# Kernel tuning notes

Hardware: AMD Instinct MI355X
Metric: run time of the kernel (lower is better)

The kernel has to match this reference:

```python
import jax, jax.numpy as jnp
import numpy as np

B, N, D, C = 2, 65536, 128, 128          # batch, n_entries, input_dim, channel_dim
DEG, N_ACTIVE, STRIDE = 16, 4096, 16     # ring-neighbor sparse structure


def _build_indices():
    """Replicates the original module's Python intersection loops exactly,
    flattening them into (src_i, src_j, pair_out) gather/scatter index arrays.
    k[:, e, :] = sum_m a[:, i_th[m], :] * b[:, j_th[m], :] for each write slot e.
    Each slot e is written exactly once, so scatter-add == the original set."""
    neigh = [[] for _ in range(N)]
    for t in range(N_ACTIVE):
        i = t * STRIDE
        neigh[i] = [((t + dlt) % N_ACTIVE) * STRIDE for dlt in range(1, DEG + 1)]
    src_i, src_j, out = [], [], []
    e = 0
    for i in range(N):
        if not neigh[i]:
            continue
        i_element = list(neigh[i]) + [i]
        i_set = set(i_element)
        for j in neigh[i]:
            j_list = neigh[j]
            j_set = set(j_list)
            j_th = [m for m in j_list if m in i_set]      # order of j's list
            i_th = [m for m in i_element if m in j_set]   # order of i_element
            for ai, bi in zip(i_th, j_th):
                src_i.append(ai)
                src_j.append(bi)
                out.append(e)
            e += 1
    return (np.asarray(src_i, np.int32), np.asarray(src_j, np.int32),
            np.asarray(out, np.int32))


def setup_inputs() -> dict:
    key = jax.random.key(0)
    ks = jax.random.split(key, 8)
    s = 1.0 / np.sqrt(D)
    src_i, src_j, pair_out = _build_indices()
    return {
        "x": jax.random.normal(ks[0], (B, N, D), jnp.float32),
        "ln_in_w": jnp.ones((D,), jnp.float32),
        "ln_in_b": jnp.zeros((D,), jnp.float32),
        "Wla": jax.random.normal(ks[1], (C, D), jnp.float32) * s,
        "bla": jnp.zeros((C,), jnp.float32),
        "Wga": jax.random.normal(ks[2], (C, D), jnp.float32) * s,
        "bga": jnp.zeros((C,), jnp.float32),
        "Wlb": jax.random.normal(ks[3], (C, D), jnp.float32) * s,
        "blb": jnp.zeros((C,), jnp.float32),
        "Wgb": jax.random.normal(ks[4], (C, D), jnp.float32) * s,
        "bgb": jnp.zeros((C,), jnp.float32),
        "ln_o_w": jnp.ones((C,), jnp.float32),
        "ln_o_b": jnp.zeros((C,), jnp.float32),
        "Wgo": jax.random.normal(ks[5], (D, D), jnp.float32) * s,
        "bgo": jnp.zeros((D,), jnp.float32),
        "Wlo": jax.random.normal(ks[6], (D, C), jnp.float32) * s,
        "blo": jnp.zeros((D,), jnp.float32),
        "src_i": jnp.asarray(src_i),
        "src_j": jnp.asarray(src_j),
        "pair_out": jnp.asarray(pair_out),
    }


def _layernorm(x, w, b, eps=1e-5):
    mu = jnp.mean(x, axis=-1, keepdims=True)
    var = jnp.mean(jnp.square(x - mu), axis=-1, keepdims=True)
    return (x - mu) * jax.lax.rsqrt(var + eps) * w + b


def reference(x, ln_in_w, ln_in_b, Wla, bla, Wga, bga, Wlb, blb, Wgb, bgb,
              ln_o_w, ln_o_b, Wgo, bgo, Wlo, blo, src_i, src_j, pair_out):
    xn = _layernorm(x, ln_in_w, ln_in_b)                              # [B,N,D]
    a = jax.nn.sigmoid(xn @ Wga.T + bga) * (xn @ Wla.T + bla)         # [B,N,C]
    b = jax.nn.sigmoid(xn @ Wgb.T + bgb) * (xn @ Wlb.T + blb)         # [B,N,C]
    # triangular update: gather-multiply-sum-scatter over precomputed pairs
    prod = a[:, src_i, :] * b[:, src_j, :]                            # [B,P,C]
    k = jnp.zeros_like(a).at[:, pair_out, :].add(prod)                # [B,N,C]
    out = jax.nn.sigmoid(xn @ Wgo.T + bgo) * (_layernorm(k, ln_o_w, ln_o_b) @ Wlo.T + blo)
    return out
```

## Files before the change

kernel.cpp:

```cpp
#include <hip/hip_runtime.h>


#define BB 2
#define NN 65536
#define DD 128
#define CC 128
#define NA 4096
#define STR 16
#define WSZ 16384

typedef short short8v __attribute__((ext_vector_type(8)));
typedef __bf16 bf16x8 __attribute__((ext_vector_type(8)));
typedef _Float16 f16x2 __attribute__((ext_vector_type(2)));
typedef _Float16 f16x8 __attribute__((ext_vector_type(8)));
typedef __fp16 fp16x2 __attribute__((ext_vector_type(2)));
typedef float f32x4 __attribute__((ext_vector_type(4)));
typedef float f32x2 __attribute__((ext_vector_type(2)));

__device__ __forceinline__ float sigf(float v) { return 1.0f / (1.0f + __expf(-v)); }
__device__ __forceinline__ short nbf(float f) {
    union { __bf16 h; short s; } u; u.h = (__bf16)f; return u.s;
}
__device__ __forceinline__ bf16x8 s2b(short8v s) {
    union { short8v s; bf16x8 b; } u; u.s = s; return u.b;
}
__device__ __forceinline__ f16x2 pkh(float a, float b) {
    union { fp16x2 p; f16x2 f; } u; u.p = __builtin_amdgcn_cvt_pkrtz(a, b); return u.f;
}

__global__ __launch_bounds__(256)
void kern_wcvt(const float* __restrict__ Wla, const float* __restrict__ Wga,
               const float* __restrict__ Wlb, const float* __restrict__ Wgb,
               const float* __restrict__ Wgo, const float* __restrict__ Wlo,
               const float* __restrict__ lnw, const float* __restrict__ lnb,
               const float* __restrict__ lnow, const float* __restrict__ lnob,
               const float* __restrict__ bla, const float* __restrict__ bga,
               const float* __restrict__ blb, const float* __restrict__ bgb,
               const float* __restrict__ bgo, const float* __restrict__ blo,
               short* __restrict__ wbf, float* __restrict__ vtab)
{
    const int b = blockIdx.x;
    if (b < 64) {
        const int i  = b * 256 + threadIdx.x;
        const int ch = i >> 7, d = i & 127;
        const int pos = ((ch >> 4) * 4 + (d >> 5)) * 512
                      + ((((d >> 3) & 3) * 16 + (ch & 15)) * 8) + (d & 7);
        const float wi = lnw[d], wo = lnow[d];
        wbf[pos]           = nbf(Wla[i] * wi);
        wbf[WSZ + pos]     = nbf(Wga[i] * wi);
        wbf[2 * WSZ + pos] = nbf(Wlb[i] * wi);
        wbf[3 * WSZ + pos] = nbf(Wgb[i] * wi);
        wbf[4 * WSZ + pos] = nbf(Wgo[i] * wi);
        wbf[5 * WSZ + pos] = nbf(Wlo[i] * wo);
    } else {
        const int t = (b - 64) * 256 + threadIdx.x;
        const int m = t >> 7, c = t & 127;
        const float* Wr = (m == 0) ? Wla : (m == 1) ? Wga : (m == 2) ? Wlb
                        : (m == 3) ? Wgb : (m == 4) ? Wgo : Wlo;
        const float* bb = (m == 5) ? lnob : lnb;
        const float* bi = (m == 0) ? bla : (m == 1) ? bga : (m == 2) ? blb
                        : (m == 3) ? bgb : (m == 4) ? bgo : blo;
        const float* row = Wr + (size_t)c * DD;
        float acc = 0.f;
        for (int d = 0; d < DD; d += 4) {
            const f32x4 w4 = *(const f32x4*)(row + d);
            const f32x4 b4 = *(const f32x4*)(bb + d);
            acc += w4[0]*b4[0] + w4[1]*b4[1] + w4[2]*b4[2] + w4[3]*b4[3];
        }
        vtab[m * 128 + c] = acc + bi[c];
    }
}

__global__ __launch_bounds__(256)
void kern_ab(const float* __restrict__ x, const short* __restrict__ wbf,
             const float* __restrict__ vtab, float* __restrict__ cbuf)
{
    const int wv    = threadIdx.x >> 6;
    const int l     = threadIdx.x & 63;
    const int bid   = blockIdx.x * 4 + wv;
    const int batch = bid >> 9;
    const int t0    = ((bid & 511) >> 1) << 4;
    const int nt0   = (bid & 1) * 4;
    const int lr    = l & 15;
    const int q     = l >> 4;
    const int fl    = l * 8;

    const float* xr = x + ((size_t)batch * NN + (size_t)(t0 + lr) * STR) * DD + q * 8;
    f32x4 v[4][2];
    #pragma unroll
    for (int kk = 0; kk < 4; ++kk) {
        v[kk][0] = *(const f32x4*)(xr + kk * 32);
        v[kk][1] = *(const f32x4*)(xr + kk * 32 + 4);
    }
    float s = 0.f, ss = 0.f;
    #pragma unroll
    for (int kk = 0; kk < 4; ++kk)
        #pragma unroll
        for (int h = 0; h < 2; ++h)
            #pragma unroll
            for (int j = 0; j < 4; ++j) { const float f = v[kk][h][j]; s += f; ss += f * f; }
    s += __shfl_xor(s, 16); ss += __shfl_xor(ss, 16);
    s += __shfl_xor(s, 32); ss += __shfl_xor(ss, 32);
    const float mu = s * (1.0f / 128.0f);
    const float rs = rsqrtf(ss * (1.0f / 128.0f) - mu * mu + 1e-5f);
    const float p  = -mu * rs;

    bf16x8 af[4];
    #pragma unroll
    for (int kk = 0; kk < 4; ++kk) {
        short8v t;
        #pragma unroll
        for (int j = 0; j < 4; ++j) {
            t[j]     = nbf(v[kk][0][j] * rs + p);
            t[4 + j] = nbf(v[kk][1][j] * rs + p);
        }
        af[kk] = s2b(t);
    }

    const short* wla = wbf;
    const short* wga = wbf + WSZ;
    const short* wlb = wbf + 2 * WSZ;
    const short* wgb = wbf + 3 * WSZ;

    #pragma unroll
    for (int nt = 0; nt < 4; ++nt) {
        const int col  = (nt0 + nt) * 16 + lr;
        const int base = ((nt0 + nt) * 4) * 512 + fl;
        f32x4 ala = {0.f,0.f,0.f,0.f}, aga = {0.f,0.f,0.f,0.f};
        f32x4 alb = {0.f,0.f,0.f,0.f}, agb = {0.f,0.f,0.f,0.f};
        #pragma unroll
        for (int kk = 0; kk < 4; ++kk) {
            const int o = base + kk * 512;
            ala = __builtin_amdgcn_mfma_f32_16x16x32_bf16(af[kk], *(const bf16x8*)(wla + o), ala, 0, 0, 0);
            aga = __builtin_amdgcn_mfma_f32_16x16x32_bf16(af[kk], *(const bf16x8*)(wga + o), aga, 0, 0, 0);
            alb = __builtin_amdgcn_mfma_f32_16x16x32_bf16(af[kk], *(const bf16x8*)(wlb + o), alb, 0, 0, 0);
            agb = __builtin_amdgcn_mfma_f32_16x16x32_bf16(af[kk], *(const bf16x8*)(wgb + o), agb, 0, 0, 0);
        }
        const float vla = vtab[col], vga = vtab[128 + col];
        const float vlb = vtab[256 + col], vgb = vtab[384 + col];
        #pragma unroll
        for (int r = 0; r < 4; ++r) {
            const float av = sigf(aga[r] + vga) * (ala[r] + vla);
            const float bv = sigf(agb[r] + vgb) * (alb[r] + vlb);
            cbuf[((size_t)batch * NA + t0 + q * 4 + r) * CC + col] = av * bv;
        }
    }
}

__global__ __launch_bounds__(256)
void kern_out(const float* __restrict__ x, const short* __restrict__ wbf,
              const float* __restrict__ vtab, const float* __restrict__ cbuf,
              float* __restrict__ out)
{
    __shared__ _Float16 kls[4][16][136];
    const int bid = blockIdx.x;
    const int swz = (bid & 7) * 256 + (bid >> 3);
    const int wv  = threadIdx.x >> 6;
    const int l   = threadIdx.x & 63;
    const int gw  = swz * 4 + wv;
    const int batch = gw >> 12;
    const int t     = gw & 4095;
    const int row0  = t * 16;

    const int lr = l & 15, lk = l >> 4;
    const int fl = l * 8;

    const float* xr = x + ((size_t)batch * NN + row0 + lr) * DD + lk * 8;
    f32x4 v[4][2];
    #pragma unroll
    for (int kk = 0; kk < 4; ++kk) {
        v[kk][0] = *(const f32x4*)(xr + kk * 32);
        v[kk][1] = *(const f32x4*)(xr + kk * 32 + 4);
    }

    const int c2 = l * 2;
    f32x2 cv[15];
    #pragma unroll
    for (int sx = 14; sx >= 0; --sx)
        cv[sx] = *(const f32x2*)(cbuf + ((size_t)batch * NA + ((t + sx + 2) & (NA - 1))) * CC + c2);

    {
        f16x2 z = {(_Float16)0.f, (_Float16)0.f};
        *(f16x2*)&kls[wv][15][c2] = z;
        float s0 = 0.f, s1 = 0.f;
        #pragma unroll
        for (int sx = 14; sx >= 0; --sx) {
            s0 += cv[sx][0]; s1 += cv[sx][1];
            *(f16x2*)&kls[wv][sx][c2] = pkh(s0, s1);
        }
    }

    bf16x8 afx[4];
    {
        float s = 0.f, ss = 0.f;
        #pragma unroll
        for (int kk = 0; kk < 4; ++kk)
            #pragma unroll
            for (int h = 0; h < 2; ++h)
                #pragma unroll
                for (int j = 0; j < 4; ++j) { const float f = v[kk][h][j]; s += f; ss += f * f; }
        s += __shfl_xor(s, 16); ss += __shfl_xor(ss, 16);
        s += __shfl_xor(s, 32); ss += __shfl_xor(ss, 32);
        const float mu = s * (1.0f / 128.0f);
        const float rs = rsqrtf(ss * (1.0f / 128.0f) - mu * mu + 1e-5f);
        const float p  = -mu * rs;
        #pragma unroll
        for (int kk = 0; kk < 4; ++kk) {
            short8v o;
            #pragma unroll
            for (int j = 0; j < 4; ++j) {
                o[j]     = nbf(v[kk][0][j] * rs + p);
                o[4 + j] = nbf(v[kk][1][j] * rs + p);
            }
            afx[kk] = s2b(o);
        }
    }

    bf16x8 afk[4];
    {
        f16x8 kraw[4];
        #pragma unroll
        for (int kk = 0; kk < 4; ++kk)
            kraw[kk] = *(const f16x8*)&kls[wv][lr][kk * 32 + lk * 8];
        float ks = 0.f, kss = 0.f;
        #pragma unroll
        for (int kk = 0; kk < 4; ++kk)
            #pragma unroll
            for (int j = 0; j < 8; ++j) { const float f = (float)kraw[kk][j]; ks += f; kss += f * f; }
        ks += __shfl_xor(ks, 16); kss += __shfl_xor(kss, 16);
        ks += __shfl_xor(ks, 32); kss += __shfl_xor(kss, 32);
        const float kmu = ks * (1.0f / 128.0f);
        const float krs = rsqrtf(kss * (1.0f / 128.0f) - kmu * kmu + 1e-5f);
        const float kp  = -kmu * krs;
        #pragma unroll
        for (int kk = 0; kk < 4; ++kk) {
            short8v o;
            #pragma unroll
            for (int j = 0; j < 8; ++j)
                o[j] = nbf((float)kraw[kk][j] * krs + kp);
            afk[kk] = s2b(o);
        }
    }

    const short* wgo = wbf + 4 * WSZ;
    const short* wlo = wbf + 5 * WSZ;
    const float* vgo = vtab + 4 * 128;
    const float* vlo = vtab + 5 * 128;
    #pragma unroll
    for (int nt = 0; nt < 8; ++nt) {
        f32x4 ag = {0.f,0.f,0.f,0.f}, ah = {0.f,0.f,0.f,0.f};
        #pragma unroll
        for (int kk = 0; kk < 4; ++kk) {
            const int o = (nt * 4 + kk) * 512 + fl;
            ag = __builtin_amdgcn_mfma_f32_16x16x32_bf16(afx[kk], *(const bf16x8*)(wgo + o), ag, 0, 0, 0);
            ah = __builtin_amdgcn_mfma_f32_16x16x32_bf16(afk[kk], *(const bf16x8*)(wlo + o), ah, 0, 0, 0);
        }
        const int   col = nt * 16 + lr;
        const float vg  = vgo[col];
        const float vl  = vlo[col];
        #pragma unroll
        for (int r = 0; r < 4; ++r) {
            const size_t rowa = (size_t)batch * NN + row0 + lk * 4 + r;
            out[rowa * DD + col] = sigf(ag[r] + vg) * (ah[r] + vl);
        }
    }
}

extern "C" void kernel_launch(void* const* d_in, const int* in_sizes, int n_in,
                              void* d_out, int out_size, void* d_ws, size_t ws_size,
                              hipStream_t stream)
{
    const float* x    = (const float*)d_in[0];
    const float* lnw  = (const float*)d_in[1];
    const float* lnb  = (const float*)d_in[2];
    const float* Wla  = (const float*)d_in[3];
    const float* bla  = (const float*)d_in[4];
    const float* Wga  = (const float*)d_in[5];
    const float* bga  = (const float*)d_in[6];
    const float* Wlb  = (const float*)d_in[7];
    const float* blb  = (const float*)d_in[8];
    const float* Wgb  = (const float*)d_in[9];
    const float* bgb  = (const float*)d_in[10];
    const float* lnow = (const float*)d_in[11];
    const float* lnob = (const float*)d_in[12];
    const float* Wgo  = (const float*)d_in[13];
    const float* bgo  = (const float*)d_in[14];
    const float* Wlo  = (const float*)d_in[15];
    const float* blo  = (const float*)d_in[16];

    float* cbuf = (float*)d_ws;
    short* wbf  = (short*)((char*)d_ws + (size_t)BB * NA * CC * 4);
    float* vtab = (float*)((char*)wbf + 6 * WSZ * sizeof(short));
    float* out  = (float*)d_out;

    hipLaunchKernelGGL(kern_wcvt, dim3(67), dim3(256), 0, stream,
                       Wla, Wga, Wlb, Wgb, Wgo, Wlo,
                       lnw, lnb, lnow, lnob,
                       bla, bga, blb, bgb, bgo, blo, wbf, vtab);
    hipLaunchKernelGGL(kern_ab, dim3(BB * 128), dim3(256), 0, stream,
                       x, wbf, vtab, cbuf);
    hipLaunchKernelGGL(kern_out, dim3(BB * 1024), dim3(256), 0, stream,
                       x, wbf, vtab, cbuf, out);
}
```

Baseline: 53.26 us.

## Stage output weights in LDS and process two row tiles per wave

kern_out now has each wave handle two 16-row tiles, so each block covers 128 rows and the grid is halved. The Wgo/Wlo bf16 weights are staged through shared memory in four double-loaded chunks instead of being read from global memory per MFMA. This amortizes weight loads across twice as many rows and across all waves of a block. The cost is more registers, extra __syncthreads barriers and fewer blocks, which may reduce occupancy and latency hiding.

```diff
diff --git a/kernel.cpp b/kernel.cpp
--- a/kernel.cpp
+++ b/kernel.cpp
@@ -152,46 +152,53 @@
               const float* __restrict__ vtab, const float* __restrict__ cbuf,
               float* __restrict__ out)
 {
+    __shared__ short    wsh[8192];
     __shared__ _Float16 kls[4][16][136];
-    const int bid = blockIdx.x;
-    const int swz = (bid & 7) * 256 + (bid >> 3);
-    const int wv  = threadIdx.x >> 6;
-    const int l   = threadIdx.x & 63;
-    const int gw  = swz * 4 + wv;
-    const int batch = gw >> 12;
-    const int t     = gw & 4095;
-    const int row0  = t * 16;
-
+    const int bid   = blockIdx.x;
+    const int swz   = (bid & 7) * 128 + (bid >> 3);
+    const int batch = swz >> 9;
+    const int ibb   = swz & 511;
+    const int row0  = ibb * 128;
+    const int t0    = ibb * 8;
+
+    const int tid = threadIdx.x;
+    const int wv = tid >> 6, l = tid & 63;
     const int lr = l & 15, lk = l >> 4;
     const int fl = l * 8;
 
-    const float* xr = x + ((size_t)batch * NN + row0 + lr) * DD + lk * 8;
-    f32x4 v[4][2];
-    #pragma unroll
-    for (int kk = 0; kk < 4; ++kk) {
-        v[kk][0] = *(const f32x4*)(xr + kk * 32);
-        v[kk][1] = *(const f32x4*)(xr + kk * 32 + 4);
-    }
-
-    const int c2 = l * 2;
-    f32x2 cv[15];
-    #pragma unroll
-    for (int sx = 14; sx >= 0; --sx)
-        cv[sx] = *(const f32x2*)(cbuf + ((size_t)batch * NA + ((t + sx + 2) & (NA - 1))) * CC + c2);
-
-    {
-        f16x2 z = {(_Float16)0.f, (_Float16)0.f};
-        *(f16x2*)&kls[wv][15][c2] = z;
-        float s0 = 0.f, s1 = 0.f;
-        #pragma unroll
-        for (int sx = 14; sx >= 0; --sx) {
-            s0 += cv[sx][0]; s1 += cv[sx][1];
-            *(f16x2*)&kls[wv][sx][c2] = pkh(s0, s1);
-        }
-    }
-
-    bf16x8 afx[4];
-    {
+    const short* wgo = wbf + 4 * WSZ;
+    const short* wlo = wbf + 5 * WSZ;
+    const float* vgo = vtab + 4 * 128;
+    const float* vlo = vtab + 5 * 128;
+
+    const int soff0 = tid * 8;
+    const int soff1 = (256 + tid) * 8;
+
+    short8v st[4];
+    st[0] = *(const short8v*)(wgo + soff0);
+    st[1] = *(const short8v*)(wgo + soff1);
+    st[2] = *(const short8v*)(wlo + soff0);
+    st[3] = *(const short8v*)(wlo + soff1);
+
+    bf16x8 afx[2], dummy_init; (void)dummy_init;
+    bf16x8 afx2[2][4], afk[2][4];
+
+    #pragma unroll
+    for (int g = 0; g < 2; ++g) {
+        const float* xr = x + ((size_t)batch * NN + row0 + wv * 32 + g * 16 + lr) * DD + lk * 8;
+        f32x4 v[4][2];
+        #pragma unroll
+        for (int kk = 0; kk < 4; ++kk) {
+            v[kk][0] = *(const f32x4*)(xr + kk * 32);
+            v[kk][1] = *(const f32x4*)(xr + kk * 32 + 4);
+        }
+        const int c2 = l * 2;
+        const int t  = t0 + wv * 2 + g;
+        f32x2 cv[15];
+        #pragma unroll
+        for (int sx = 14; sx >= 0; --sx)
+            cv[sx] = *(const f32x2*)(cbuf + ((size_t)batch * NA + ((t + sx + 2) & (NA - 1))) * CC + c2);
+
         float s = 0.f, ss = 0.f;
         #pragma unroll
         for (int kk = 0; kk < 4; ++kk)
@@ -212,56 +219,92 @@
                 o[j]     = nbf(v[kk][0][j] * rs + p);
                 o[4 + j] = nbf(v[kk][1][j] * rs + p);
             }
-            afx[kk] = s2b(o);
-        }
-    }
-
-    bf16x8 afk[4];
-    {
-        f16x8 kraw[4];
-        #pragma unroll
-        for (int kk = 0; kk < 4; ++kk)
-            kraw[kk] = *(const f16x8*)&kls[wv][lr][kk * 32 + lk * 8];
-        float ks = 0.f, kss = 0.f;
-        #pragma unroll
-        for (int kk = 0; kk < 4; ++kk)
-            #pragma unroll
-            for (int j = 0; j < 8; ++j) { const float f = (float)kraw[kk][j]; ks += f; kss += f * f; }
-        ks += __shfl_xor(ks, 16); kss += __shfl_xor(kss, 16);
-        ks += __shfl_xor(ks, 32); kss += __shfl_xor(kss, 32);
-        const float kmu = ks * (1.0f / 128.0f);
-        const float krs = rsqrtf(kss * (1.0f / 128.0f) - kmu * kmu + 1e-5f);
-        const float kp  = -kmu * krs;
-        #pragma unroll
-        for (int kk = 0; kk < 4; ++kk) {
-            short8v o;
-            #pragma unroll
-            for (int j = 0; j < 8; ++j)
-                o[j] = nbf((float)kraw[kk][j] * krs + kp);
-            afk[kk] = s2b(o);
-        }
-    }
-
-    const short* wgo = wbf + 4 * WSZ;
-    const short* wlo = wbf + 5 * WSZ;
-    const float* vgo = vtab + 4 * 128;
-    const float* vlo = vtab + 5 * 128;
-    #pragma unroll
-    for (int nt = 0; nt < 8; ++nt) {
-        f32x4 ag = {0.f,0.f,0.f,0.f}, ah = {0.f,0.f,0.f,0.f};
-        #pragma unroll
-        for (int kk = 0; kk < 4; ++kk) {
-            const int o = (nt * 4 + kk) * 512 + fl;
-            ag = __builtin_amdgcn_mfma_f32_16x16x32_bf16(afx[kk], *(const bf16x8*)(wgo + o), ag, 0, 0, 0);
-            ah = __builtin_amdgcn_mfma_f32_16x16x32_bf16(afk[kk], *(const bf16x8*)(wlo + o), ah, 0, 0, 0);
-        }
-        const int   col = nt * 16 + lr;
-        const float vg  = vgo[col];
-        const float vl  = vlo[col];
-        #pragma unroll
-        for (int r = 0; r < 4; ++r) {
-            const size_t rowa = (size_t)batch * NN + row0 + lk * 4 + r;
-            out[rowa * DD + col] = sigf(ag[r] + vg) * (ah[r] + vl);
+            afx2[g][kk] = s2b(o);
+        }
+
+        {
+            f16x2 z = {(_Float16)0.f, (_Float16)0.f};
+            *(f16x2*)&kls[wv][15][c2] = z;
+            float s0 = 0.f, s1 = 0.f;
+            #pragma unroll
+            for (int sx = 14; sx >= 0; --sx) {
+                s0 += cv[sx][0]; s1 += cv[sx][1];
+                *(f16x2*)&kls[wv][sx][c2] = pkh(s0, s1);
+            }
+        }
+        {
+            f16x8 kraw[4];
+            #pragma unroll
+            for (int kk = 0; kk < 4; ++kk)
+                kraw[kk] = *(const f16x8*)&kls[wv][lr][kk * 32 + lk * 8];
+            float ks = 0.f, kss = 0.f;
+            #pragma unroll
+            for (int kk = 0; kk < 4; ++kk)
+                #pragma unroll
+                for (int j = 0; j < 8; ++j) { const float f = (float)kraw[kk][j]; ks += f; kss += f * f; }
+            ks += __shfl_xor(ks, 16); kss += __shfl_xor(kss, 16);
+            ks += __shfl_xor(ks, 32); kss += __shfl_xor(kss, 32);
+            const float kmu = ks * (1.0f / 128.0f);
+            const float krs = rsqrtf(kss * (1.0f / 128.0f) - kmu * kmu + 1e-5f);
+            const float kp  = -kmu * krs;
+            #pragma unroll
+            for (int kk = 0; kk < 4; ++kk) {
+                short8v o;
+                #pragma unroll
+                for (int j = 0; j < 8; ++j)
+                    o[j] = nbf((float)kraw[kk][j] * krs + kp);
+                afk[g][kk] = s2b(o);
+            }
+        }
+    }
+    (void)afx;
+
+    *(short8v*)&wsh[soff0]        = st[0];
+    *(short8v*)&wsh[soff1]        = st[1];
+    *(short8v*)&wsh[4096 + soff0] = st[2];
+    *(short8v*)&wsh[4096 + soff1] = st[3];
+    __syncthreads();
+
+    #pragma unroll
+    for (int sg = 0; sg < 4; ++sg) {
+        if (sg < 3) {
+            const int gofs = (sg + 1) * 4096;
+            st[0] = *(const short8v*)(wgo + gofs + soff0);
+            st[1] = *(const short8v*)(wgo + gofs + soff1);
+            st[2] = *(const short8v*)(wlo + gofs + soff0);
+            st[3] = *(const short8v*)(wlo + gofs + soff1);
+        }
+        #pragma unroll
+        for (int ntl = 0; ntl < 2; ++ntl) {
+            const int nt = sg * 2 + ntl;
+            f32x4 ag0 = {0.f,0.f,0.f,0.f}, ag1 = {0.f,0.f,0.f,0.f};
+            f32x4 ah0 = {0.f,0.f,0.f,0.f}, ah1 = {0.f,0.f,0.f,0.f};
+            #pragma unroll
+            for (int kk = 0; kk < 4; ++kk) {
+                const bf16x8 bg = *(const bf16x8*)&wsh[ntl * 2048 + kk * 512 + fl];
+                const bf16x8 bh = *(const bf16x8*)&wsh[4096 + ntl * 2048 + kk * 512 + fl];
+                ag0 = __builtin_amdgcn_mfma_f32_16x16x32_bf16(afx2[0][kk], bg, ag0, 0, 0, 0);
+                ag1 = __builtin_amdgcn_mfma_f32_16x16x32_bf16(afx2[1][kk], bg, ag1, 0, 0, 0);
+                ah0 = __builtin_amdgcn_mfma_f32_16x16x32_bf16(afk[0][kk], bh, ah0, 0, 0, 0);
+                ah1 = __builtin_amdgcn_mfma_f32_16x16x32_bf16(afk[1][kk], bh, ah1, 0, 0, 0);
+            }
+            const int   col = nt * 16 + lr;
+            const float vg  = vgo[col];
+            const float vl  = vlo[col];
+            #pragma unroll
+            for (int r = 0; r < 4; ++r) {
+                const size_t rowa = (size_t)batch * NN + row0 + wv * 32 + lk * 4 + r;
+                out[rowa * DD + col]        = sigf(ag0[r] + vg) * (ah0[r] + vl);
+                out[(rowa + 16) * DD + col] = sigf(ag1[r] + vg) * (ah1[r] + vl);
+            }
+        }
+        if (sg < 3) {
+            __syncthreads();
+            *(short8v*)&wsh[soff0]        = st[0];
+            *(short8v*)&wsh[soff1]        = st[1];
+            *(short8v*)&wsh[4096 + soff0] = st[2];
+            *(short8v*)&wsh[4096 + soff1] = st[3];
+            __syncthreads();
         }
     }
 }
@@ -299,6 +342,6 @@
                        bla, bga, blb, bgb, bgo, blo, wbf, vtab);
     hipLaunchKernelGGL(kern_ab, dim3(BB * 128), dim3(256), 0, stream,
                        x, wbf, vtab, cbuf);
-    hipLaunchKernelGGL(kern_out, dim3(BB * 1024), dim3(256), 0, stream,
+    hipLaunchKernelGGL(kern_out, dim3(BB * 512), dim3(256), 0, stream,
                        x, wbf, vtab, cbuf, out);
 }
```

Measured after the change: 55.32 us. 3.9% more time.
